# Kernel optimization log

Hardware: AMD Instinct MI355X
Metric: run time of the kernel (lower is better)

The kernel has to match this reference:

```python
import jax, jax.numpy as jnp
import numpy as np

N_NODES = 16384
HIST_LEN = 50
EMBED_DIM = 64
N_USERS = 100000
N_ITEMS = 100000
N_RATINGS = 6


def setup_inputs() -> dict:
    key = jax.random.key(0)
    ks = jax.random.split(key, 16)
    d = EMBED_DIM
    inp = {
        "nodes": jax.random.randint(ks[0], (N_NODES,), 0, N_USERS),
        "hist_items": jax.random.randint(ks[1], (N_NODES, HIST_LEN), 0, N_ITEMS),
        "hist_ratings": jax.random.randint(ks[2], (N_NODES, HIST_LEN), 0, N_RATINGS),
        # at least one valid neighbor per node (original code assumes non-empty history)
        "hist_len": jax.random.randint(ks[3], (N_NODES,), 1, HIST_LEN + 1),
        # embedding tables
        "u2e_w": jax.random.normal(ks[4], (N_USERS, d), jnp.float32) * 0.02,
        "i2e_w": jax.random.normal(ks[5], (N_ITEMS, d), jnp.float32) * 0.02,
        "r2e_w": jax.random.normal(ks[6], (N_RATINGS, d), jnp.float32) * 0.02,
        # 2-layer MLP (torch Linear: y = x @ W.T + b, W is [out, in])
        "w1_w": jax.random.normal(ks[7], (d, 2 * d), jnp.float32) * (1.0 / np.sqrt(2 * d)),
        "w1_b": jnp.zeros((d,), jnp.float32),
        "w2_w": jax.random.normal(ks[8], (d, d), jnp.float32) * (1.0 / np.sqrt(d)),
        "w2_b": jnp.zeros((d,), jnp.float32),
        # GraphRec attention MLP
        "att1_w": jax.random.normal(ks[9], (d, 2 * d), jnp.float32) * (1.0 / np.sqrt(2 * d)),
        "att1_b": jnp.zeros((d,), jnp.float32),
        "att2_w": jax.random.normal(ks[10], (d, d), jnp.float32) * (1.0 / np.sqrt(d)),
        "att2_b": jnp.zeros((d,), jnp.float32),
        "att3_w": jax.random.normal(ks[11], (1, d), jnp.float32) * (1.0 / np.sqrt(d)),
        "att3_b": jnp.zeros((1,), jnp.float32),
    }
    return inp


def reference(nodes, hist_items, hist_ratings, hist_len,
              u2e_w, i2e_w, r2e_w,
              w1_w, w1_b, w2_w, w2_b,
              att1_w, att1_b, att2_w, att2_b, att3_w, att3_b):
    L = hist_items.shape[1]
    u_rep = u2e_w[nodes]                               # [N, d]
    p_embed = i2e_w[hist_items]                        # [N, L, d]
    r_embed = r2e_w[hist_ratings]                      # [N, L, d]
    x = jnp.concatenate([p_embed, r_embed], axis=-1)   # [N, L, 2d]
    x = jax.nn.relu(x @ w1_w.T + w1_b)                 # [N, L, d]
    o = jax.nn.relu(x @ w2_w.T + w2_b)                 # [N, L, d]
    # attention of each neighbor rep against the user rep
    u_b = jnp.broadcast_to(u_rep[:, None, :], o.shape) # [N, L, d]
    a = jnp.concatenate([o, u_b], axis=-1)             # [N, L, 2d]
    a = jax.nn.relu(a @ att1_w.T + att1_b)
    a = jax.nn.relu(a @ att2_w.T + att2_b)
    scores = (a @ att3_w.T + att3_b)[..., 0]           # [N, L]
    mask = jnp.arange(L)[None, :] < hist_len[:, None]  # valid (ragged) positions
    scores = jnp.where(mask, scores, -jnp.inf)
    att = jax.nn.softmax(scores, axis=-1)              # [N, L]
    return jnp.einsum('nl,nld->nd', att, o)            # [N, d]
```

## Files before the change

### kernel.cpp

```cpp
#include <hip/hip_runtime.h>
#include <hip/hip_fp16.h>

#define HIST 50
#define WPB 8

typedef __fp16 hf;
typedef __fp16 hf2 __attribute__((ext_vector_type(2)));
typedef __fp16 h8  __attribute__((ext_vector_type(8)));
typedef float  f4  __attribute__((ext_vector_type(4)));

union U32H2 { unsigned u; hf2 h; };
__device__ __forceinline__ unsigned h2u(hf2 h){ U32H2 c; c.h=h; return c.u; }
__device__ __forceinline__ hf2 pkrtz(float a,float b){ return __builtin_amdgcn_cvt_pkrtz(a,b); }

__device__ __forceinline__ h8 mk8(hf2 a, hf2 b, hf2 c, hf2 d){
    h8 r; r[0]=a[0]; r[1]=a[1]; r[2]=b[0]; r[3]=b[1]; r[4]=c[0]; r[5]=c[1]; r[6]=d[0]; r[7]=d[1]; return r;
}
__device__ __forceinline__ h8 ldfrag(const float* W, long row, int kb){
    const float4 v0 = *(const float4*)(W + row + kb);
    const float4 v1 = *(const float4*)(W + row + kb + 4);
    return mk8(pkrtz(v0.x,v0.y), pkrtz(v0.z,v0.w), pkrtz(v1.x,v1.y), pkrtz(v1.z,v1.w));
}
__device__ __forceinline__ f4 mfma16(h8 a, h8 b, f4 c){
    return __builtin_amdgcn_mfma_f32_16x16x32_f16(a,b,c,0,0,0);
}
__device__ __forceinline__ f4 relu4(f4 v){
    v[0]=fmaxf(v[0],0.f); v[1]=fmaxf(v[1],0.f); v[2]=fmaxf(v[2],0.f); v[3]=fmaxf(v[3],0.f); return v;
}
__device__ __forceinline__ void wsync(){
    asm volatile("s_waitcnt lgkmcnt(0)" ::: "memory");
    __builtin_amdgcn_sched_barrier(0);
}

__device__ __forceinline__ void store_ct(unsigned short* base, const f4* acc, int lane){
    const int m0 = (lane >> 4) * 4;
    const int ci = lane & 15;
    #pragma unroll
    for (int nt = 0; nt < 4; ++nt){
        const int c = 16*nt + ci;
        #pragma unroll
        for (int r = 0; r < 4; ++r){
            const int m    = m0 + r;
            const int gp   = (c >> 3) ^ (m & 7);
            const int byte = m*128 + gp*16 + ((2*c) & 15);
            *(hf*)((char*)base + byte) = (hf)acc[nt][r];
        }
    }
}
__device__ __forceinline__ h8 read_af(const unsigned short* base, int lane, int kt){
    const int row  = lane & 15;
    const int gp   = (4*kt + (lane>>4)) ^ (row & 7);
    const int byte = row*128 + gp*16;
    return *(const h8*)((const char*)base + byte);
}

__global__ __launch_bounds__(512, 2)
void ue_v8(const int* __restrict__ nodes, const int* __restrict__ hitems,
           const int* __restrict__ hrat, const int* __restrict__ hlen,
           const float* __restrict__ u2e, const float* __restrict__ i2e,
           const float* __restrict__ r2e,
           const float* __restrict__ w1w, const float* __restrict__ w1b,
           const float* __restrict__ w2w, const float* __restrict__ w2b,
           const float* __restrict__ a1w, const float* __restrict__ a1b,
           const float* __restrict__ a2w, const float* __restrict__ a2b,
           const float* __restrict__ a3w, const float* __restrict__ a3b,
           float* __restrict__ out, int n_nodes)
{
    const int tid  = threadIdx.x;
    const int lane = tid & 63;
    const int wid  = tid >> 6;
    const int nidx = lane & 15;
    const int kg   = lane >> 4;

    __shared__ __align__(16) unsigned short wlds[40*512];
    __shared__ __align__(16) unsigned short xfer[WPB][16*64];
    __shared__ __align__(16) float uax[WPB][64];
    __shared__ __align__(16) float ubl[WPB][64];
    __shared__ int ihs[WPB][HIST];
    __shared__ int rhs[WPB][HIST];

    for (int f = tid; f < 40*64; f += blockDim.x) {
        const int blk = f >> 6, l = f & 63;
        const float* src; int ld, kt, nt;
        if (blk < 16)      { kt = blk>>2;      nt = blk&3;      src = w1w; ld = 128; }
        else if (blk < 24) { kt = (blk-16)>>2; nt = (blk-16)&3; src = w2w; ld = 64;  }
        else if (blk < 32) { kt = (blk-24)>>2; nt = (blk-24)&3; src = a1w; ld = 128; }
        else               { kt = (blk-32)>>2; nt = (blk-32)&3; src = a2w; ld = 64;  }
        const int nrow = 16*nt + (l & 15);
        const int kcol = 32*kt + 8*(l >> 4);
        *(h8*)&wlds[blk*512 + l*8] = ldfrag(src, (long)nrow*ld, kcol);
    }
    __syncthreads();

    #define BF(base,kt,nt) (*(const h8*)&wlds[((base)+(kt)*4+(nt))*512 + lane*8])

    float b1c[4], b2c[4], ab2c[4], a3c[4];
    #pragma unroll
    for (int nt = 0; nt < 4; ++nt){
        b1c[nt]  = w1b[16*nt + nidx];
        b2c[nt]  = w2b[16*nt + nidx];
        ab2c[nt] = a2b[16*nt + nidx];
        a3c[nt]  = a3w[16*nt + nidx];
    }
    const float ab1r = a1b[lane];
    const float NEG_INF = -__builtin_inff();

    for (int n = blockIdx.x * WPB + wid; n < n_nodes; n += gridDim.x * WPB) {
        const int node = nodes[n];
        const int hl   = hlen[n];

        uax[wid][lane] = u2e[(long)node * 64 + lane];
        if (lane < HIST){ ihs[wid][lane] = hitems[n*HIST+lane]; rhs[wid][lane] = hrat[n*HIST+lane]; }
        wsync();

        float u0 = ab1r, u1 = 0.f, u2 = 0.f, u3 = 0.f;
        #pragma unroll
        for (int t = 0; t < 16; ++t) {
            const float4 v = *(const float4*)(a1w + (long)lane*128 + 64 + 4*t);
            u0 = fmaf(v.x, uax[wid][4*t+0], u0);
            u1 = fmaf(v.y, uax[wid][4*t+1], u1);
            u2 = fmaf(v.z, uax[wid][4*t+2], u2);
            u3 = fmaf(v.w, uax[wid][4*t+3], u3);
        }
        ubl[wid][lane] = (u0 + u1) + (u2 + u3);
        wsync();
        float ubc[4];
        #pragma unroll
        for (int nt = 0; nt < 4; ++nt) ubc[nt] = ubl[wid][16*nt + nidx];

        float m_run = NEG_INF, run_sum = 0.f;
        float outacc[4] = {0.f, 0.f, 0.f, 0.f};

        const int tiles = (hl + 15) >> 4;
        for (int t = 0; t < tiles; ++t) {
            int p = t*16 + nidx; if (p >= hl) p = hl - 1;
            const long irow = (long)ihs[wid][p] * 64;
            const long rrow = (long)rhs[wid][p] * 64;
            const int  kb   = 8 * kg;
            const h8 Xf0 = ldfrag(i2e, irow, kb);
            const h8 Xf1 = ldfrag(i2e, irow, 32 + kb);
            const h8 Xf2 = ldfrag(r2e, rrow, kb);
            const h8 Xf3 = ldfrag(r2e, rrow, 32 + kb);

            f4 acc[4];
            #pragma unroll
            for (int nt = 0; nt < 4; ++nt){
                f4 c = { b1c[nt], b1c[nt], b1c[nt], b1c[nt] };
                c = mfma16(Xf0, BF(0,0,nt), c);
                c = mfma16(Xf1, BF(0,1,nt), c);
                c = mfma16(Xf2, BF(0,2,nt), c);
                c = mfma16(Xf3, BF(0,3,nt), c);
                acc[nt] = relu4(c);
            }
            store_ct(xfer[wid], acc, lane);
            wsync();
            const h8 yf0 = read_af(xfer[wid], lane, 0), yf1 = read_af(xfer[wid], lane, 1);

            f4 occ[4];
            #pragma unroll
            for (int nt = 0; nt < 4; ++nt){
                f4 c = { b2c[nt], b2c[nt], b2c[nt], b2c[nt] };
                c = mfma16(yf0, BF(16,0,nt), c);
                c = mfma16(yf1, BF(16,1,nt), c);
                occ[nt] = relu4(c);
            }
            store_ct(xfer[wid], occ, lane);
            wsync();
            const h8 of0 = read_af(xfer[wid], lane, 0), of1 = read_af(xfer[wid], lane, 1);

            #pragma unroll
            for (int nt = 0; nt < 4; ++nt){
                f4 c = { ubc[nt], ubc[nt], ubc[nt], ubc[nt] };
                c = mfma16(of0, BF(24,0,nt), c);
                c = mfma16(of1, BF(24,1,nt), c);
                acc[nt] = relu4(c);
            }
            store_ct(xfer[wid], acc, lane);
            wsync();
            const h8 af0 = read_af(xfer[wid], lane, 0), af1 = read_af(xfer[wid], lane, 1);

            #pragma unroll
            for (int nt = 0; nt < 4; ++nt){
                f4 c = { ab2c[nt], ab2c[nt], ab2c[nt], ab2c[nt] };
                c = mfma16(af0, BF(32,0,nt), c);
                c = mfma16(af1, BF(32,1,nt), c);
                acc[nt] = relu4(c);
            }

            float sv0 = 0.f, sv1 = 0.f, sv2 = 0.f, sv3 = 0.f;
            #pragma unroll
            for (int nt = 0; nt < 4; ++nt){
                sv0 = fmaf(acc[nt][0], a3c[nt], sv0);
                sv1 = fmaf(acc[nt][1], a3c[nt], sv1);
                sv2 = fmaf(acc[nt][2], a3c[nt], sv2);
                sv3 = fmaf(acc[nt][3], a3c[nt], sv3);
            }
            #pragma unroll
            for (int off = 1; off <= 8; off <<= 1){
                sv0 += __shfl_xor(sv0, off);
                sv1 += __shfl_xor(sv1, off);
                sv2 += __shfl_xor(sv2, off);
                sv3 += __shfl_xor(sv3, off);
            }

            const int base = t*16 + kg*4;
            const bool v0 = base+0 < hl, v1 = base+1 < hl, v2 = base+2 < hl, v3 = base+3 < hl;
            float tmax = fmaxf(fmaxf(v0 ? sv0 : NEG_INF, v1 ? sv1 : NEG_INF),
                               fmaxf(v2 ? sv2 : NEG_INF, v3 ? sv3 : NEG_INF));
            tmax = fmaxf(tmax, __shfl_xor(tmax, 16));
            tmax = fmaxf(tmax, __shfl_xor(tmax, 32));
            const float m_new = fmaxf(m_run, tmax);
            const float fs = expf(m_run - m_new);
            const float w0 = v0 ? expf(sv0 - m_new) : 0.f;
            const float w1 = v1 ? expf(sv1 - m_new) : 0.f;
            const float w2 = v2 ? expf(sv2 - m_new) : 0.f;
            const float w3 = v3 ? expf(sv3 - m_new) : 0.f;
            float wsum = (w0 + w1) + (w2 + w3);
            float cp[4];
            #pragma unroll
            for (int nt = 0; nt < 4; ++nt)
                cp[nt] = ((w0*occ[nt][0] + w1*occ[nt][1]) + (w2*occ[nt][2] + w3*occ[nt][3]));
            wsum += __shfl_xor(wsum, 16); wsum += __shfl_xor(wsum, 32);
            #pragma unroll
            for (int nt = 0; nt < 4; ++nt){
                cp[nt] += __shfl_xor(cp[nt], 16);
                cp[nt] += __shfl_xor(cp[nt], 32);
            }
            run_sum = run_sum * fs + wsum;
            #pragma unroll
            for (int nt = 0; nt < 4; ++nt) outacc[nt] = outacc[nt] * fs + cp[nt];
            m_run = m_new;
        }

        const float inv = 1.f / run_sum;
        if (kg == 0){
            #pragma unroll
            for (int nt = 0; nt < 4; ++nt)
                out[(long)n * 64 + 16*nt + nidx] = outacc[nt] * inv;
        }
    }
    #undef BF
}

extern "C" void kernel_launch(void* const* d_in, const int* in_sizes, int n_in,
                              void* d_out, int out_size, void* d_ws, size_t ws_size,
                              hipStream_t stream) {
    const int*   nodes  = (const int*)d_in[0];
    const int*   hitems = (const int*)d_in[1];
    const int*   hrat   = (const int*)d_in[2];
    const int*   hlenp  = (const int*)d_in[3];
    const float* u2e    = (const float*)d_in[4];
    const float* i2e    = (const float*)d_in[5];
    const float* r2e    = (const float*)d_in[6];
    const float* w1w    = (const float*)d_in[7];
    const float* w1b    = (const float*)d_in[8];
    const float* w2w    = (const float*)d_in[9];
    const float* w2b    = (const float*)d_in[10];
    const float* a1w    = (const float*)d_in[11];
    const float* a1b    = (const float*)d_in[12];
    const float* a2w    = (const float*)d_in[13];
    const float* a2b    = (const float*)d_in[14];
    const float* a3w    = (const float*)d_in[15];
    const float* a3b    = (const float*)d_in[16];
    float* out = (float*)d_out;

    const int n_nodes = in_sizes[0];
    const int blocks  = 512;
    ue_v8<<<dim3(blocks), dim3(512), 0, stream>>>(
        nodes, hitems, hrat, hlenp, u2e, i2e, r2e,
        w1w, w1b, w2w, w2b, a1w, a1b, a2w, a2b, a3w, a3b,
        out, n_nodes);
}
```

Before: 110.7 us.

## Process 32-neighbor tiles per wave and halve waves per block

Each wave now handles two 16-row sub-tiles per iteration, 32 history positions instead of 16. All gathers are issued up front and the four MLP stages run across both sub-tiles between each LDS sync. This halves the sync and softmax-rescale overhead per neighbor and exposes more memory-level parallelism. Block size drops from 512 to 256 threads (4 waves) with the same 512-block grid. That cuts total resident waves, adds register pressure from the doubled fragments, and wastes more padded work for short histories.

```diff
diff --git a/kernel.cpp b/kernel.cpp
--- a/kernel.cpp
+++ b/kernel.cpp
@@ -2,7 +2,7 @@
 #include <hip/hip_fp16.h>
 
 #define HIST 50
-#define WPB 8
+#define WPB 4
 
 typedef __fp16 hf;
 typedef __fp16 hf2 __attribute__((ext_vector_type(2)));
@@ -32,8 +32,8 @@
     __builtin_amdgcn_sched_barrier(0);
 }
 
-__device__ __forceinline__ void store_ct(unsigned short* base, const f4* acc, int lane){
-    const int m0 = (lane >> 4) * 4;
+__device__ __forceinline__ void store_ct(unsigned short* base, const f4* acc, int lane, int pt){
+    const int m0 = pt*16 + (lane >> 4) * 4;
     const int ci = lane & 15;
     #pragma unroll
     for (int nt = 0; nt < 4; ++nt){
@@ -47,15 +47,15 @@
         }
     }
 }
-__device__ __forceinline__ h8 read_af(const unsigned short* base, int lane, int kt){
-    const int row  = lane & 15;
+__device__ __forceinline__ h8 read_af(const unsigned short* base, int lane, int kt, int pt){
+    const int row  = pt*16 + (lane & 15);
     const int gp   = (4*kt + (lane>>4)) ^ (row & 7);
     const int byte = row*128 + gp*16;
     return *(const h8*)((const char*)base + byte);
 }
 
-__global__ __launch_bounds__(512, 2)
-void ue_v8(const int* __restrict__ nodes, const int* __restrict__ hitems,
+__global__ __launch_bounds__(256, 2)
+void ue_v9(const int* __restrict__ nodes, const int* __restrict__ hitems,
            const int* __restrict__ hrat, const int* __restrict__ hlen,
            const float* __restrict__ u2e, const float* __restrict__ i2e,
            const float* __restrict__ r2e,
@@ -73,7 +73,7 @@
     const int kg   = lane >> 4;
 
     __shared__ __align__(16) unsigned short wlds[40*512];
-    __shared__ __align__(16) unsigned short xfer[WPB][16*64];
+    __shared__ __align__(16) unsigned short xfer[WPB][32*64];
     __shared__ __align__(16) float uax[WPB][64];
     __shared__ __align__(16) float ubl[WPB][64];
     __shared__ int ihs[WPB][HIST];
@@ -131,95 +131,125 @@
         float m_run = NEG_INF, run_sum = 0.f;
         float outacc[4] = {0.f, 0.f, 0.f, 0.f};
 
-        const int tiles = (hl + 15) >> 4;
+        const int tiles = (hl + 31) >> 5;
         for (int t = 0; t < tiles; ++t) {
-            int p = t*16 + nidx; if (p >= hl) p = hl - 1;
-            const long irow = (long)ihs[wid][p] * 64;
-            const long rrow = (long)rhs[wid][p] * 64;
-            const int  kb   = 8 * kg;
-            const h8 Xf0 = ldfrag(i2e, irow, kb);
-            const h8 Xf1 = ldfrag(i2e, irow, 32 + kb);
-            const h8 Xf2 = ldfrag(r2e, rrow, kb);
-            const h8 Xf3 = ldfrag(r2e, rrow, 32 + kb);
-
-            f4 acc[4];
-            #pragma unroll
-            for (int nt = 0; nt < 4; ++nt){
-                f4 c = { b1c[nt], b1c[nt], b1c[nt], b1c[nt] };
-                c = mfma16(Xf0, BF(0,0,nt), c);
-                c = mfma16(Xf1, BF(0,1,nt), c);
-                c = mfma16(Xf2, BF(0,2,nt), c);
-                c = mfma16(Xf3, BF(0,3,nt), c);
-                acc[nt] = relu4(c);
-            }
-            store_ct(xfer[wid], acc, lane);
+            h8 Xf[2][4];
+            #pragma unroll
+            for (int pt = 0; pt < 2; ++pt){
+                int p = t*32 + pt*16 + nidx; if (p >= hl) p = hl - 1;
+                const long irow = (long)ihs[wid][p] * 64;
+                const long rrow = (long)rhs[wid][p] * 64;
+                const int  kb   = 8 * kg;
+                Xf[pt][0] = ldfrag(i2e, irow, kb);
+                Xf[pt][1] = ldfrag(i2e, irow, 32 + kb);
+                Xf[pt][2] = ldfrag(r2e, rrow, kb);
+                Xf[pt][3] = ldfrag(r2e, rrow, 32 + kb);
+            }
+
+            #pragma unroll
+            for (int pt = 0; pt < 2; ++pt){
+                f4 acc[4];
+                #pragma unroll
+                for (int nt = 0; nt < 4; ++nt){
+                    f4 c = { b1c[nt], b1c[nt], b1c[nt], b1c[nt] };
+                    c = mfma16(Xf[pt][0], BF(0,0,nt), c);
+                    c = mfma16(Xf[pt][1], BF(0,1,nt), c);
+                    c = mfma16(Xf[pt][2], BF(0,2,nt), c);
+                    c = mfma16(Xf[pt][3], BF(0,3,nt), c);
+                    acc[nt] = relu4(c);
+                }
+                store_ct(xfer[wid], acc, lane, pt);
+            }
             wsync();
-            const h8 yf0 = read_af(xfer[wid], lane, 0), yf1 = read_af(xfer[wid], lane, 1);
-
-            f4 occ[4];
-            #pragma unroll
-            for (int nt = 0; nt < 4; ++nt){
-                f4 c = { b2c[nt], b2c[nt], b2c[nt], b2c[nt] };
-                c = mfma16(yf0, BF(16,0,nt), c);
-                c = mfma16(yf1, BF(16,1,nt), c);
-                occ[nt] = relu4(c);
-            }
-            store_ct(xfer[wid], occ, lane);
+
+            f4 occ[2][4];
+            #pragma unroll
+            for (int pt = 0; pt < 2; ++pt){
+                const h8 yf0 = read_af(xfer[wid], lane, 0, pt);
+                const h8 yf1 = read_af(xfer[wid], lane, 1, pt);
+                #pragma unroll
+                for (int nt = 0; nt < 4; ++nt){
+                    f4 c = { b2c[nt], b2c[nt], b2c[nt], b2c[nt] };
+                    c = mfma16(yf0, BF(16,0,nt), c);
+                    c = mfma16(yf1, BF(16,1,nt), c);
+                    occ[pt][nt] = relu4(c);
+                }
+                store_ct(xfer[wid], occ[pt], lane, pt);
+            }
             wsync();
-            const h8 of0 = read_af(xfer[wid], lane, 0), of1 = read_af(xfer[wid], lane, 1);
-
-            #pragma unroll
-            for (int nt = 0; nt < 4; ++nt){
-                f4 c = { ubc[nt], ubc[nt], ubc[nt], ubc[nt] };
-                c = mfma16(of0, BF(24,0,nt), c);
-                c = mfma16(of1, BF(24,1,nt), c);
-                acc[nt] = relu4(c);
-            }
-            store_ct(xfer[wid], acc, lane);
+
+            #pragma unroll
+            for (int pt = 0; pt < 2; ++pt){
+                const h8 of0 = read_af(xfer[wid], lane, 0, pt);
+                const h8 of1 = read_af(xfer[wid], lane, 1, pt);
+                f4 acc[4];
+                #pragma unroll
+                for (int nt = 0; nt < 4; ++nt){
+                    f4 c = { ubc[nt], ubc[nt], ubc[nt], ubc[nt] };
+                    c = mfma16(of0, BF(24,0,nt), c);
+                    c = mfma16(of1, BF(24,1,nt), c);
+                    acc[nt] = relu4(c);
+                }
+                store_ct(xfer[wid], acc, lane, pt);
+            }
             wsync();
-            const h8 af0 = read_af(xfer[wid], lane, 0), af1 = read_af(xfer[wid], lane, 1);
-
-            #pragma unroll
-            for (int nt = 0; nt < 4; ++nt){
-                f4 c = { ab2c[nt], ab2c[nt], ab2c[nt], ab2c[nt] };
-                c = mfma16(af0, BF(32,0,nt), c);
-                c = mfma16(af1, BF(32,1,nt), c);
-                acc[nt] = relu4(c);
-            }
-
-            float sv0 = 0.f, sv1 = 0.f, sv2 = 0.f, sv3 = 0.f;
-            #pragma unroll
-            for (int nt = 0; nt < 4; ++nt){
-                sv0 = fmaf(acc[nt][0], a3c[nt], sv0);
-                sv1 = fmaf(acc[nt][1], a3c[nt], sv1);
-                sv2 = fmaf(acc[nt][2], a3c[nt], sv2);
-                sv3 = fmaf(acc[nt][3], a3c[nt], sv3);
-            }
-            #pragma unroll
-            for (int off = 1; off <= 8; off <<= 1){
-                sv0 += __shfl_xor(sv0, off);
-                sv1 += __shfl_xor(sv1, off);
-                sv2 += __shfl_xor(sv2, off);
-                sv3 += __shfl_xor(sv3, off);
-            }
-
-            const int base = t*16 + kg*4;
-            const bool v0 = base+0 < hl, v1 = base+1 < hl, v2 = base+2 < hl, v3 = base+3 < hl;
-            float tmax = fmaxf(fmaxf(v0 ? sv0 : NEG_INF, v1 ? sv1 : NEG_INF),
-                               fmaxf(v2 ? sv2 : NEG_INF, v3 ? sv3 : NEG_INF));
+
+            float w8[2][4];
+            float tmax = NEG_INF;
+            #pragma unroll
+            for (int pt = 0; pt < 2; ++pt){
+                const h8 af0 = read_af(xfer[wid], lane, 0, pt);
+                const h8 af1 = read_af(xfer[wid], lane, 1, pt);
+                f4 acc[4];
+                #pragma unroll
+                for (int nt = 0; nt < 4; ++nt){
+                    f4 c = { ab2c[nt], ab2c[nt], ab2c[nt], ab2c[nt] };
+                    c = mfma16(af0, BF(32,0,nt), c);
+                    c = mfma16(af1, BF(32,1,nt), c);
+                    acc[nt] = relu4(c);
+                }
+                float sv0 = 0.f, sv1 = 0.f, sv2 = 0.f, sv3 = 0.f;
+                #pragma unroll
+                for (int nt = 0; nt < 4; ++nt){
+                    sv0 = fmaf(acc[nt][0], a3c[nt], sv0);
+                    sv1 = fmaf(acc[nt][1], a3c[nt], sv1);
+                    sv2 = fmaf(acc[nt][2], a3c[nt], sv2);
+                    sv3 = fmaf(acc[nt][3], a3c[nt], sv3);
+                }
+                #pragma unroll
+                for (int off = 1; off <= 8; off <<= 1){
+                    sv0 += __shfl_xor(sv0, off);
+                    sv1 += __shfl_xor(sv1, off);
+                    sv2 += __shfl_xor(sv2, off);
+                    sv3 += __shfl_xor(sv3, off);
+                }
+                const int base = t*32 + pt*16 + kg*4;
+                w8[pt][0] = (base+0 < hl) ? sv0 : NEG_INF;
+                w8[pt][1] = (base+1 < hl) ? sv1 : NEG_INF;
+                w8[pt][2] = (base+2 < hl) ? sv2 : NEG_INF;
+                w8[pt][3] = (base+3 < hl) ? sv3 : NEG_INF;
+                tmax = fmaxf(tmax, fmaxf(fmaxf(w8[pt][0], w8[pt][1]), fmaxf(w8[pt][2], w8[pt][3])));
+            }
             tmax = fmaxf(tmax, __shfl_xor(tmax, 16));
             tmax = fmaxf(tmax, __shfl_xor(tmax, 32));
             const float m_new = fmaxf(m_run, tmax);
             const float fs = expf(m_run - m_new);
-            const float w0 = v0 ? expf(sv0 - m_new) : 0.f;
-            const float w1 = v1 ? expf(sv1 - m_new) : 0.f;
-            const float w2 = v2 ? expf(sv2 - m_new) : 0.f;
-            const float w3 = v3 ? expf(sv3 - m_new) : 0.f;
-            float wsum = (w0 + w1) + (w2 + w3);
+            float wsum = 0.f;
+            #pragma unroll
+            for (int pt = 0; pt < 2; ++pt)
+                #pragma unroll
+                for (int r = 0; r < 4; ++r){
+                    w8[pt][r] = (w8[pt][r] == NEG_INF) ? 0.f : expf(w8[pt][r] - m_new);
+                    wsum += w8[pt][r];
+                }
             float cp[4];
             #pragma unroll
-            for (int nt = 0; nt < 4; ++nt)
-                cp[nt] = ((w0*occ[nt][0] + w1*occ[nt][1]) + (w2*occ[nt][2] + w3*occ[nt][3]));
+            for (int nt = 0; nt < 4; ++nt){
+                cp[nt] = ((w8[0][0]*occ[0][nt][0] + w8[0][1]*occ[0][nt][1]) +
+                          (w8[0][2]*occ[0][nt][2] + w8[0][3]*occ[0][nt][3])) +
+                         ((w8[1][0]*occ[1][nt][0] + w8[1][1]*occ[1][nt][1]) +
+                          (w8[1][2]*occ[1][nt][2] + w8[1][3]*occ[1][nt][3]));
+            }
             wsum += __shfl_xor(wsum, 16); wsum += __shfl_xor(wsum, 32);
             #pragma unroll
             for (int nt = 0; nt < 4; ++nt){
@@ -266,7 +296,7 @@
 
     const int n_nodes = in_sizes[0];
     const int blocks  = 512;
-    ue_v8<<<dim3(blocks), dim3(512), 0, stream>>>(
+    ue_v9<<<dim3(blocks), dim3(256), 0, stream>>>(
         nodes, hitems, hrat, hlenp, u2e, i2e, r2e,
         w1w, w1b, w2w, w2b, a1w, a1b, a2w, a2b, a3w, a3b,
         out, n_nodes);
```

After: 100.3 us (median of 2 runs). -9.3%, faster.
